# Kernel optimization log

Measured on AMD Instinct MI355X. Metric: run time of the kernel, lower is better.

Reference implementation:

```python
import jax, jax.numpy as jnp
import numpy as np


def _bilinear_sample_zeros(img, px, py):
    """Bilinear sample img [B,C,H,W] at pixel coords px,py [B,...], zeros padding,
    align_corners=True semantics (coords are direct pixel indices)."""
    B, C, H, W = img.shape
    shp = px.shape
    px_f = px.reshape(B, -1)
    py_f = py.reshape(B, -1)
    x0 = jnp.floor(px_f)
    y0 = jnp.floor(py_f)
    fx = px_f - x0  # fractional offsets
    fy = py_f - y0
    x0i = x0.astype(jnp.int32)
    y0i = y0.astype(jnp.int32)
    img_flat = img.reshape(B, C, H * W)

    def corner(xi, yi, w):
        valid = ((xi >= 0) & (xi < W) & (yi >= 0) & (yi < H)).astype(img.dtype)
        xc = jnp.clip(xi, 0, W - 1)
        yc = jnp.clip(yi, 0, H - 1)
        idx = (yc * W + xc)[:, None, :]  # [B,1,N]
        v = jnp.take_along_axis(img_flat, idx, axis=2)  # [B,C,N]
        return v * (w * valid)[:, None, :]

    out = (corner(x0i, y0i, (1.0 - fx) * (1.0 - fy))
           + corner(x0i + 1, y0i, fx * (1.0 - fy))
           + corner(x0i, y0i + 1, (1.0 - fx) * fy)
           + corner(x0i + 1, y0i + 1, fx * fy))
    return out.reshape((B, C) + shp[1:])


def setup_inputs() -> dict:
    key = jax.random.key(0)
    k1, k2, k3 = jax.random.split(key, 3)
    B, C, H, W, D = 2, 32, 128, 256, 48
    x = jax.random.normal(k1, (B, C, H, W), dtype=jnp.float32)
    y = jax.random.normal(k2, (B, C, H, W), dtype=jnp.float32)
    disp = jax.random.uniform(k3, (B, D, H, W), dtype=jnp.float32) * 64.0
    return {"x": x, "y": y, "disp_range_samples": disp, "ndisp": D}


def reference(x, y, disp_range_samples, ndisp):
    B, C, H, W = x.shape
    # pixel coords of the warp: sample right image at (w - disparity, h)
    mw = jnp.arange(W, dtype=x.dtype).reshape(1, 1, 1, W)
    mh = jnp.arange(H, dtype=x.dtype).reshape(1, 1, H, 1)
    px = mw - disp_range_samples                       # [B, D, H, W]
    py = jnp.broadcast_to(mh, px.shape)                # [B, D, H, W]
    warped = _bilinear_sample_zeros(y, px, py)         # [B, C, D, H, W]
    # correlation mode: elementwise multiply with left features, mean over channels
    cost = (warped * x[:, :, None, :, :]).mean(axis=1)  # [B, D, H, W]
    return cost
```

## Files before the change

### kernel.cpp

```cpp
#include <hip/hip_runtime.h>

#define BB 2
#define CC 32
#define HH 128
#define WW 256
#define DD 48
#define HW (HH * WW)
#define WT 128
#define HALO 64
#define YR (HALO + WT)


__device__ __forceinline__ void ldg16_lds(const float* g, float* l) {
  __builtin_amdgcn_global_load_lds(
      (const __attribute__((address_space(1))) void*)g,
      (__attribute__((address_space(3))) void*)l, 16, 0, 0);
}

__global__ __launch_bounds__(512, 4) void cost_volume_kernel(
    const float* __restrict__ x, const float* __restrict__ y,
    const float* __restrict__ disp, float* __restrict__ out) {
  __shared__ float xs[CC * WT];
  __shared__ float ys[CC * YR];
  __shared__ float corr[65 * WT];

  const int bx = blockIdx.x;
  const int tile = bx & 1;
  const int h = (bx >> 1) & (HH - 1);
  const int b = bx >> 8;
  const int wt0 = tile << 7;
  const int tid = threadIdx.x;

  const int gbase = (b * CC * HH + h) * WW;

#pragma unroll
  for (int k = 0; k < 2; ++k) {
    int t4 = tid + (k << 9);
    int c = t4 >> 5;
    int w4 = (t4 & 31) << 2;
    ldg16_lds(x + gbase + c * HW + wt0 + w4, &xs[t4 << 2]);
  }
  if (tile) {
#pragma unroll
    for (int k = 0; k < 3; ++k) {
      int t4 = tid + (k << 9);
      int c = t4 / 48;
      int j4 = t4 - c * 48;
      ldg16_lds(y + gbase + c * HW + (wt0 - HALO) + (j4 << 2), &ys[t4 << 2]);
    }
  } else {
#pragma unroll
    for (int k = 0; k < 3; ++k) {
      int t4 = tid + (k << 9);
      int c = t4 / 48;
      int j = (t4 - c * 48) << 2;
      float4 v = make_float4(0.f, 0.f, 0.f, 0.f);
      if (j >= HALO) v = *(const float4*)(y + gbase + c * HW + (j - HALO));
      *(float4*)&ys[c * YR + j] = v;
    }
  }
  const int dobase = (b * DD * HH + h) * WW + wt0;
  float dreg[12];
#pragma unroll
  for (int k = 0; k < 12; ++k) {
    int idx = tid + (k << 9);
    int d = idx >> 7;
    int w = idx & (WT - 1);
    dreg[k] = disp[dobase + d * HW + w];
  }
  __syncthreads();

  const int lane = tid & 63;
  const int wid = tid >> 6;
  const int half = lane >> 5;
  const int w0 = (lane & 31) << 2;
  const int g = wid + (half << 3);
  const int A = HALO + w0 - (g << 2) - 4;

  float acc[4][4];
#pragma unroll
  for (int sl = 0; sl < 4; ++sl)
#pragma unroll
    for (int wj = 0; wj < 4; ++wj) acc[sl][wj] = 0.f;
  float a64[4] = {0.f, 0.f, 0.f, 0.f};

#pragma unroll 4
  for (int c = 0; c < CC; ++c) {
    float4 xv = *(const float4*)&xs[c * WT + w0];
    float4 wv0 = *(const float4*)&ys[c * YR + A];
    float4 wv1 = *(const float4*)&ys[c * YR + A + 4];
    float win[8] = {wv0.x, wv0.y, wv0.z, wv0.w, wv1.x, wv1.y, wv1.z, wv1.w};
    float xr[4] = {xv.x, xv.y, xv.z, xv.w};
#pragma unroll
    for (int sl = 0; sl < 4; ++sl)
#pragma unroll
      for (int wj = 0; wj < 4; ++wj)
        acc[sl][wj] = fmaf(xr[wj], win[4 + wj - sl], acc[sl][wj]);
    if (wid == 0) {
      float4 yv = *(const float4*)&ys[c * YR + w0];
      a64[0] = fmaf(xr[0], yv.x, a64[0]);
      a64[1] = fmaf(xr[1], yv.y, a64[1]);
      a64[2] = fmaf(xr[2], yv.z, a64[2]);
      a64[3] = fmaf(xr[3], yv.w, a64[3]);
    }
  }
#pragma unroll
  for (int sl = 0; sl < 4; ++sl)
    *(float4*)&corr[((g << 2) + sl) * WT + w0] =
        make_float4(acc[sl][0], acc[sl][1], acc[sl][2], acc[sl][3]);
  if (wid == 0 && half == 0)
    *(float4*)&corr[64 * WT + w0] = make_float4(a64[0], a64[1], a64[2], a64[3]);
  __syncthreads();

  const float inv_c = 1.0f / (float)CC;
  float* obase = out + dobase;
#pragma unroll
  for (int k = 0; k < 12; ++k) {
    int idx = tid + (k << 9);
    int d = idx >> 7;
    int w = idx & (WT - 1);
    float dv = dreg[k];
    float s0f = ceilf(dv);
    int i0 = (int)s0f;
    float fx = s0f - dv;
    int i1 = (i0 > 0) ? i0 - 1 : 0;
    float c0 = corr[i0 * WT + w];
    float c1 = corr[i1 * WT + w];
    obase[d * HW + w] = (c0 + fx * (c1 - c0)) * inv_c;
  }
}

extern "C" void kernel_launch(void* const* d_in, const int* in_sizes, int n_in,
                              void* d_out, int out_size, void* d_ws, size_t ws_size,
                              hipStream_t stream) {
  const float* x = (const float*)d_in[0];
  const float* y = (const float*)d_in[1];
  const float* disp = (const float*)d_in[2];
  float* out = (float*)d_out;
  cost_volume_kernel<<<BB * HH * 2, 512, 0, stream>>>(x, y, disp, out);
}
```

Measured before the change: 88.58 us.

## Compute correlation with 9 warp-teams of 8 shifts each, overlap disp loads

The correlation phase is remapped so that only 8 half-wave teams each compute 8 integer shifts (plus one team for shift 64), rather than all 16 groups computing 4 shifts each. Each thread reuses its x registers over more shifts and issues fewer LDS reads per FMA. The displacement global loads are moved after the compute so they overlap with the other threads' work. The tradeoff is that most of the 512 threads now sit idle during compute, so per-block compute parallelism drops. This risks a longer critical path in that phase.

```diff
diff --git a/kernel.cpp b/kernel.cpp
--- a/kernel.cpp
+++ b/kernel.cpp
@@ -59,6 +59,54 @@
       *(float4*)&ys[c * YR + j] = v;
     }
   }
+  __syncthreads();
+
+  const int team = tid >> 5;
+  const int tlane = tid & 31;
+  const int w0 = tlane << 2;
+
+  if (team < 8) {
+    float acc[8][4];
+#pragma unroll
+    for (int sl = 0; sl < 8; ++sl)
+#pragma unroll
+      for (int wj = 0; wj < 4; ++wj) acc[sl][wj] = 0.f;
+
+    const int A = HALO + w0 - (team << 3) - 8;
+#pragma unroll 4
+    for (int c = 0; c < CC; ++c) {
+      float4 xv = *(const float4*)&xs[c * WT + w0];
+      const float* yrow = &ys[c * YR];
+      float4 wv0 = *(const float4*)&yrow[A];
+      float4 wv1 = *(const float4*)&yrow[A + 4];
+      float4 wv2 = *(const float4*)&yrow[A + 8];
+      float win[12] = {wv0.x, wv0.y, wv0.z, wv0.w, wv1.x, wv1.y,
+                       wv1.z, wv1.w, wv2.x, wv2.y, wv2.z, wv2.w};
+      float xr[4] = {xv.x, xv.y, xv.z, xv.w};
+#pragma unroll
+      for (int sl = 0; sl < 8; ++sl)
+#pragma unroll
+        for (int wj = 0; wj < 4; ++wj)
+          acc[sl][wj] = fmaf(xr[wj], win[8 + wj - sl], acc[sl][wj]);
+    }
+#pragma unroll
+    for (int sl = 0; sl < 8; ++sl)
+      *(float4*)&corr[((team << 3) + sl) * WT + w0] =
+          make_float4(acc[sl][0], acc[sl][1], acc[sl][2], acc[sl][3]);
+  } else if (team == 8) {
+    float a64[4] = {0.f, 0.f, 0.f, 0.f};
+#pragma unroll 4
+    for (int c = 0; c < CC; ++c) {
+      float4 xv = *(const float4*)&xs[c * WT + w0];
+      float4 yv = *(const float4*)&ys[c * YR + w0];
+      a64[0] = fmaf(xv.x, yv.x, a64[0]);
+      a64[1] = fmaf(xv.y, yv.y, a64[1]);
+      a64[2] = fmaf(xv.z, yv.z, a64[2]);
+      a64[3] = fmaf(xv.w, yv.w, a64[3]);
+    }
+    *(float4*)&corr[64 * WT + w0] = make_float4(a64[0], a64[1], a64[2], a64[3]);
+  }
+
   const int dobase = (b * DD * HH + h) * WW + wt0;
   float dreg[12];
 #pragma unroll
@@ -68,48 +116,6 @@
     int w = idx & (WT - 1);
     dreg[k] = disp[dobase + d * HW + w];
   }
-  __syncthreads();
-
-  const int lane = tid & 63;
-  const int wid = tid >> 6;
-  const int half = lane >> 5;
-  const int w0 = (lane & 31) << 2;
-  const int g = wid + (half << 3);
-  const int A = HALO + w0 - (g << 2) - 4;
-
-  float acc[4][4];
-#pragma unroll
-  for (int sl = 0; sl < 4; ++sl)
-#pragma unroll
-    for (int wj = 0; wj < 4; ++wj) acc[sl][wj] = 0.f;
-  float a64[4] = {0.f, 0.f, 0.f, 0.f};
-
-#pragma unroll 4
-  for (int c = 0; c < CC; ++c) {
-    float4 xv = *(const float4*)&xs[c * WT + w0];
-    float4 wv0 = *(const float4*)&ys[c * YR + A];
-    float4 wv1 = *(const float4*)&ys[c * YR + A + 4];
-    float win[8] = {wv0.x, wv0.y, wv0.z, wv0.w, wv1.x, wv1.y, wv1.z, wv1.w};
-    float xr[4] = {xv.x, xv.y, xv.z, xv.w};
-#pragma unroll
-    for (int sl = 0; sl < 4; ++sl)
-#pragma unroll
-      for (int wj = 0; wj < 4; ++wj)
-        acc[sl][wj] = fmaf(xr[wj], win[4 + wj - sl], acc[sl][wj]);
-    if (wid == 0) {
-      float4 yv = *(const float4*)&ys[c * YR + w0];
-      a64[0] = fmaf(xr[0], yv.x, a64[0]);
-      a64[1] = fmaf(xr[1], yv.y, a64[1]);
-      a64[2] = fmaf(xr[2], yv.z, a64[2]);
-      a64[3] = fmaf(xr[3], yv.w, a64[3]);
-    }
-  }
-#pragma unroll
-  for (int sl = 0; sl < 4; ++sl)
-    *(float4*)&corr[((g << 2) + sl) * WT + w0] =
-        make_float4(acc[sl][0], acc[sl][1], acc[sl][2], acc[sl][3]);
-  if (wid == 0 && half == 0)
-    *(float4*)&corr[64 * WT + w0] = make_float4(a64[0], a64[1], a64[2], a64[3]);
   __syncthreads();
 
   const float inv_c = 1.0f / (float)CC;
```

After: 85.85 us. 3.1% less time.
